# Kernel tuning notes

Hardware: AMD Instinct MI355X
Metric: run time of the kernel (lower is better)

## Reference

```python
import jax, jax.numpy as jnp
import numpy as np

N_NODES = 100000
N_EDGES = 1600000
NUM_FEATURES = 128
DIM = 64
NUM_GRAPHS = 64


def setup_inputs() -> dict:
    key = jax.random.key(0)
    ks = jax.random.split(key, 8)
    x = jax.random.normal(ks[0], (N_NODES, NUM_FEATURES), dtype=jnp.float32)
    edge_index = jax.random.randint(ks[1], (2, N_EDGES), 0, N_NODES, dtype=jnp.int64)
    batch = jnp.sort(jax.random.randint(ks[2], (N_NODES,), 0, NUM_GRAPHS, dtype=jnp.int64))
    s = 1.0 / np.sqrt(NUM_FEATURES)
    w_lin0 = jax.random.uniform(ks[3], (NUM_FEATURES, DIM), jnp.float32, -s, s)
    b_lin0 = jnp.zeros((DIM,), jnp.float32)
    s2 = 1.0 / np.sqrt(DIM)
    w0 = jax.random.uniform(ks[4], (DIM, DIM), jnp.float32, -s2, s2)
    w1 = jax.random.uniform(ks[5], (DIM, DIM), jnp.float32, -s2, s2)
    b_cheb = jnp.zeros((DIM,), jnp.float32)
    return {"x": x, "edge_index": edge_index, "batch": batch,
            "w_lin0": w_lin0, "b_lin0": b_lin0, "w0": w0, "w1": w1, "b_cheb": b_cheb}


def reference(x, edge_index, batch, w_lin0, b_lin0, w0, w1, b_cheb):
    # out = relu(lin0(x))
    out = jax.nn.relu(x @ w_lin0 + b_lin0)  # [N, DIM]

    src, dst = edge_index[0], edge_index[1]
    n = out.shape[0]
    # ChebConv K=2, sym normalization, lambda_max=2 (PyG default):
    # scaled Laplacian L_hat = L - I = -D^{-1/2} A D^{-1/2} (diagonal cancels to 0)
    deg = jax.ops.segment_sum(jnp.ones(src.shape, out.dtype), src, num_segments=n)
    dinv = jnp.where(deg > 0, 1.0 / jnp.sqrt(jnp.where(deg > 0, deg, 1.0)), 0.0)
    norm = -dinv[src] * dinv[dst]  # [E]

    tx0 = out
    # Tx_1 = L_hat @ x : gather source features, scale, scatter-add to targets
    tx1 = jax.ops.segment_sum(norm[:, None] * out[src], dst, num_segments=n)  # [N, DIM]

    h = jax.nn.relu(tx0 @ w0 + tx1 @ w1 + b_cheb)  # [N, DIM]

    pooled = jax.ops.segment_sum(h, batch, num_segments=NUM_GRAPHS)  # [G, DIM]
    return pooled, h
```

## Files before the change

### kernel.cpp

```cpp
#include <hip/hip_runtime.h>
#include <hip/hip_bf16.h>

#define N_NODES     100000
#define N_EDGES     1600000
#define NFEAT       128
#define DIM         64
#define NGRAPHS     64

#define CAP         64

#define ROWS_PB     32
#define NB_ROWS     ((N_NODES + ROWS_PB - 1) / ROWS_PB)

__device__ __forceinline__ float bf2f(unsigned short u) {
    return __uint_as_float(((unsigned)u) << 16);
}
__device__ __forceinline__ unsigned short f2bf(float f) {
    unsigned u = __float_as_uint(f);
    u += 0x7fffu + ((u >> 16) & 1u);
    return (unsigned short)(u >> 16);
}

__global__ __launch_bounds__(256) void init_kernel(
    int* __restrict__ deg, int* __restrict__ cursor, float* __restrict__ pooled)
{
    int i = blockIdx.x * 256 + threadIdx.x;
    if (i < N_NODES) {
        deg[i] = 0;
        cursor[i] = i * CAP;
    }
    if (i < NGRAPHS * DIM) pooled[i] = 0.0f;
}

__global__ __launch_bounds__(256) void lin0_kernel(
    const float* __restrict__ x, const float* __restrict__ w,
    const float* __restrict__ b, unsigned short* __restrict__ tx0b)
{
    __shared__ float wl[NFEAT * DIM];
    for (int i = threadIdx.x; i < NFEAT * DIM; i += 256) wl[i] = w[i];
    __syncthreads();

    const int lane = threadIdx.x & 63;
    const int wv   = threadIdx.x >> 6;
    const int r0   = blockIdx.x * ROWS_PB + wv * 8;
    if (r0 >= N_NODES) return;
    const float bv = b[lane];

    float acc[8];
#pragma unroll
    for (int j = 0; j < 8; ++j) acc[j] = bv;

    for (int k4 = 0; k4 < NFEAT / 4; ++k4) {
        const int k = k4 * 4;
        float4 xv[8];
#pragma unroll
        for (int j = 0; j < 8; ++j)
            xv[j] = *(const float4*)(x + (size_t)(r0 + j) * NFEAT + k);
        float w0v = wl[(k + 0) * DIM + lane];
        float w1v = wl[(k + 1) * DIM + lane];
        float w2v = wl[(k + 2) * DIM + lane];
        float w3v = wl[(k + 3) * DIM + lane];
#pragma unroll
        for (int j = 0; j < 8; ++j) {
            acc[j] = fmaf(xv[j].x, w0v, acc[j]);
            acc[j] = fmaf(xv[j].y, w1v, acc[j]);
            acc[j] = fmaf(xv[j].z, w2v, acc[j]);
            acc[j] = fmaf(xv[j].w, w3v, acc[j]);
        }
    }
#pragma unroll
    for (int j = 0; j < 8; ++j)
        tx0b[(size_t)(r0 + j) * DIM + lane] = f2bf(fmaxf(acc[j], 0.0f));
}

__global__ __launch_bounds__(256) void csr_deg_kernel(
    const int* __restrict__ ei, int* __restrict__ deg,
    int* __restrict__ cursor, int* __restrict__ csr_src)
{
    int e = blockIdx.x * 256 + threadIdx.x;
    if (e >= N_EDGES) return;
    int s = ei[e];
    int d = ei[N_EDGES + e];
    atomicAdd(&deg[s], 1);
    int pos = atomicAdd(&cursor[d], 1);
    if (pos < d * CAP + CAP)
        csr_src[pos] = s;
}

__global__ __launch_bounds__(256) void gather_kernel(
    const int* __restrict__ csr_src, const int* __restrict__ cursor,
    const int* __restrict__ deg, const unsigned short* __restrict__ tx0b,
    unsigned short* __restrict__ tx1b)
{
    int node = blockIdx.x * 4 + (threadIdx.x >> 6);
    if (node >= N_NODES) return;
    int lane = threadIdx.x & 63;
    int sub  = lane >> 4;
    int q    = lane & 15;

    int beg = node * CAP;
    int end = cursor[node];
    if (end > beg + CAP) end = beg + CAP;

    float4 acc = make_float4(0.f, 0.f, 0.f, 0.f);
    int p = beg + sub;
    for (; p + 4 < end; p += 8) {
        int s0 = csr_src[p];
        int s1 = csr_src[p + 4];
        float d0 = rsqrtf((float)deg[s0]);
        float d1 = rsqrtf((float)deg[s1]);
        ushort4 v0 = *(const ushort4*)(tx0b + (size_t)s0 * DIM + q * 4);
        ushort4 v1 = *(const ushort4*)(tx0b + (size_t)s1 * DIM + q * 4);
        acc.x = fmaf(d0, bf2f(v0.x), acc.x);
        acc.y = fmaf(d0, bf2f(v0.y), acc.y);
        acc.z = fmaf(d0, bf2f(v0.z), acc.z);
        acc.w = fmaf(d0, bf2f(v0.w), acc.w);
        acc.x = fmaf(d1, bf2f(v1.x), acc.x);
        acc.y = fmaf(d1, bf2f(v1.y), acc.y);
        acc.z = fmaf(d1, bf2f(v1.z), acc.z);
        acc.w = fmaf(d1, bf2f(v1.w), acc.w);
    }
    if (p < end) {
        int s = csr_src[p];
        float ds = rsqrtf((float)deg[s]);
        ushort4 v = *(const ushort4*)(tx0b + (size_t)s * DIM + q * 4);
        acc.x = fmaf(ds, bf2f(v.x), acc.x);
        acc.y = fmaf(ds, bf2f(v.y), acc.y);
        acc.z = fmaf(ds, bf2f(v.z), acc.z);
        acc.w = fmaf(ds, bf2f(v.w), acc.w);
    }
#pragma unroll
    for (int off = 16; off <= 32; off <<= 1) {
        acc.x += __shfl_xor(acc.x, off, 64);
        acc.y += __shfl_xor(acc.y, off, 64);
        acc.z += __shfl_xor(acc.z, off, 64);
        acc.w += __shfl_xor(acc.w, off, 64);
    }
    if (sub == 0) {
        int dg = deg[node];
        float nd = (dg > 0) ? -rsqrtf((float)dg) : 0.0f;
        ushort4 r;
        r.x = f2bf(nd * acc.x);
        r.y = f2bf(nd * acc.y);
        r.z = f2bf(nd * acc.z);
        r.w = f2bf(nd * acc.w);
        *(ushort4*)(tx1b + (size_t)node * DIM + q * 4) = r;
    }
}

__global__ __launch_bounds__(256) void cheb_kernel(
    const unsigned short* __restrict__ tx0b, const unsigned short* __restrict__ tx1b,
    const float* __restrict__ w0, const float* __restrict__ w1,
    const float* __restrict__ b, const int* __restrict__ batch,
    float* __restrict__ pooled, float* __restrict__ h)
{
    __shared__ float w0l[DIM * DIM];
    __shared__ float w1l[DIM * DIM];
    for (int i = threadIdx.x; i < DIM * DIM; i += 256) {
        w0l[i] = w0[i];
        w1l[i] = w1[i];
    }
    __syncthreads();

    const int lane = threadIdx.x & 63;
    const int wv   = threadIdx.x >> 6;
    const int r0   = blockIdx.x * ROWS_PB + wv * 8;
    if (r0 >= N_NODES) return;
    const float bv = b[lane];

    float acc[8];
#pragma unroll
    for (int j = 0; j < 8; ++j) acc[j] = bv;

    for (int k4 = 0; k4 < DIM / 4; ++k4) {
        const int k = k4 * 4;
        float a0 = w0l[(k + 0) * DIM + lane];
        float a1 = w0l[(k + 1) * DIM + lane];
        float a2 = w0l[(k + 2) * DIM + lane];
        float a3 = w0l[(k + 3) * DIM + lane];
        float c0 = w1l[(k + 0) * DIM + lane];
        float c1 = w1l[(k + 1) * DIM + lane];
        float c2 = w1l[(k + 2) * DIM + lane];
        float c3 = w1l[(k + 3) * DIM + lane];
#pragma unroll
        for (int j = 0; j < 8; ++j) {
            ushort4 t0 = *(const ushort4*)(tx0b + (size_t)(r0 + j) * DIM + k);
            ushort4 t1 = *(const ushort4*)(tx1b + (size_t)(r0 + j) * DIM + k);
            acc[j] = fmaf(bf2f(t0.x), a0, acc[j]);
            acc[j] = fmaf(bf2f(t0.y), a1, acc[j]);
            acc[j] = fmaf(bf2f(t0.z), a2, acc[j]);
            acc[j] = fmaf(bf2f(t0.w), a3, acc[j]);
            acc[j] = fmaf(bf2f(t1.x), c0, acc[j]);
            acc[j] = fmaf(bf2f(t1.y), c1, acc[j]);
            acc[j] = fmaf(bf2f(t1.z), c2, acc[j]);
            acc[j] = fmaf(bf2f(t1.w), c3, acc[j]);
        }
    }

    float acc_pool = 0.0f;
    int cur_g = -1;
#pragma unroll
    for (int j = 0; j < 8; ++j) {
        float hv = fmaxf(acc[j], 0.0f);
        h[(size_t)(r0 + j) * DIM + lane] = hv;
        int g = batch[r0 + j];
        if (g != cur_g) {
            if (cur_g >= 0) unsafeAtomicAdd(&pooled[cur_g * DIM + lane], acc_pool);
            cur_g = g;
            acc_pool = 0.0f;
        }
        acc_pool += hv;
    }
    if (cur_g >= 0) unsafeAtomicAdd(&pooled[cur_g * DIM + lane], acc_pool);
}

extern "C" void kernel_launch(void* const* d_in, const int* in_sizes, int n_in,
                              void* d_out, int out_size, void* d_ws, size_t ws_size,
                              hipStream_t stream)
{
    const float* x      = (const float*)d_in[0];
    const int*   ei     = (const int*)d_in[1];
    const int*   batch  = (const int*)d_in[2];
    const float* w_lin0 = (const float*)d_in[3];
    const float* b_lin0 = (const float*)d_in[4];
    const float* w0     = (const float*)d_in[5];
    const float* w1     = (const float*)d_in[6];
    const float* b_cheb = (const float*)d_in[7];

    float* pooled = (float*)d_out;
    float* h      = (float*)d_out + NGRAPHS * DIM;

    char* wp = (char*)d_ws;
    unsigned short* tx0b = (unsigned short*)wp; wp += (size_t)N_NODES * DIM * sizeof(unsigned short);
    unsigned short* tx1b = (unsigned short*)wp; wp += (size_t)N_NODES * DIM * sizeof(unsigned short);
    int* deg     = (int*)wp;  wp += (size_t)N_NODES * sizeof(int);
    int* cursor  = (int*)wp;  wp += (size_t)N_NODES * sizeof(int);
    int* csr_src = (int*)wp;  wp += (size_t)N_NODES * CAP * sizeof(int);

    init_kernel<<<(N_NODES + 255) / 256, 256, 0, stream>>>(deg, cursor, pooled);

    lin0_kernel<<<NB_ROWS, 256, 0, stream>>>(x, w_lin0, b_lin0, tx0b);

    csr_deg_kernel<<<(N_EDGES + 255) / 256, 256, 0, stream>>>(ei, deg, cursor, csr_src);

    gather_kernel<<<(N_NODES + 3) / 4, 256, 0, stream>>>(csr_src, cursor, deg, tx0b, tx1b);

    cheb_kernel<<<NB_ROWS, 256, 0, stream>>>(tx0b, tx1b, w0, w1, b_cheb,
                                             batch, pooled, h);
}
```

Baseline: 517.5 us.

## Prescale tx0 by source dinv and widen gather loads to 16 bytes

A new pass multiplies each tx0 row in place by rsqrt(deg) of its source node. The gather then sums prescaled rows without reading deg[src] or doing an rsqrt per edge, and uses 16-byte loads with 8 lanes per neighbor row. The cheb kernel splits its accumulators and multiplies the tx0 part by sqrt(deg) to undo the scaling. This adds an extra read-write pass over tx0 and a second bf16 rounding of the scaled values, which could cost some accuracy.

```diff
diff --git a/kernel.cpp b/kernel.cpp
--- a/kernel.cpp
+++ b/kernel.cpp
@@ -11,6 +11,8 @@
 
 #define ROWS_PB     32
 #define NB_ROWS     ((N_NODES + ROWS_PB - 1) / ROWS_PB)
+
+typedef unsigned short ushort8v __attribute__((ext_vector_type(8)));
 
 __device__ __forceinline__ float bf2f(unsigned short u) {
     return __uint_as_float(((unsigned)u) << 16);
@@ -87,69 +89,73 @@
         csr_src[pos] = s;
 }
 
+__global__ __launch_bounds__(256) void scale_kernel(
+    const int* __restrict__ deg, unsigned short* __restrict__ tx0b)
+{
+    int t = blockIdx.x * 256 + threadIdx.x;
+    if (t >= N_NODES * DIM / 8) return;
+    int node = t >> 3;
+    int dg = deg[node];
+    float f = (dg > 0) ? rsqrtf((float)dg) : 1.0f;
+    ushort8v v = *(((const ushort8v*)tx0b) + t);
+#pragma unroll
+    for (int k = 0; k < 8; ++k) v[k] = f2bf(f * bf2f(v[k]));
+    *(((ushort8v*)tx0b) + t) = v;
+}
+
 __global__ __launch_bounds__(256) void gather_kernel(
     const int* __restrict__ csr_src, const int* __restrict__ cursor,
-    const int* __restrict__ deg, const unsigned short* __restrict__ tx0b,
+    const int* __restrict__ deg, const unsigned short* __restrict__ tx0s,
     unsigned short* __restrict__ tx1b)
 {
     int node = blockIdx.x * 4 + (threadIdx.x >> 6);
     if (node >= N_NODES) return;
     int lane = threadIdx.x & 63;
-    int sub  = lane >> 4;
-    int q    = lane & 15;
+    int sub  = lane >> 3;
+    int q    = lane & 7;
 
     int beg = node * CAP;
     int end = cursor[node];
     if (end > beg + CAP) end = beg + CAP;
 
-    float4 acc = make_float4(0.f, 0.f, 0.f, 0.f);
+    float acc[8];
+#pragma unroll
+    for (int k = 0; k < 8; ++k) acc[k] = 0.0f;
+
     int p = beg + sub;
-    for (; p + 4 < end; p += 8) {
+    for (; p + 8 < end; p += 16) {
         int s0 = csr_src[p];
-        int s1 = csr_src[p + 4];
-        float d0 = rsqrtf((float)deg[s0]);
-        float d1 = rsqrtf((float)deg[s1]);
-        ushort4 v0 = *(const ushort4*)(tx0b + (size_t)s0 * DIM + q * 4);
-        ushort4 v1 = *(const ushort4*)(tx0b + (size_t)s1 * DIM + q * 4);
-        acc.x = fmaf(d0, bf2f(v0.x), acc.x);
-        acc.y = fmaf(d0, bf2f(v0.y), acc.y);
-        acc.z = fmaf(d0, bf2f(v0.z), acc.z);
-        acc.w = fmaf(d0, bf2f(v0.w), acc.w);
-        acc.x = fmaf(d1, bf2f(v1.x), acc.x);
-        acc.y = fmaf(d1, bf2f(v1.y), acc.y);
-        acc.z = fmaf(d1, bf2f(v1.z), acc.z);
-        acc.w = fmaf(d1, bf2f(v1.w), acc.w);
+        int s1 = csr_src[p + 8];
+        ushort8v v0 = *(const ushort8v*)(tx0s + (size_t)s0 * DIM + q * 8);
+        ushort8v v1 = *(const ushort8v*)(tx0s + (size_t)s1 * DIM + q * 8);
+#pragma unroll
+        for (int k = 0; k < 8; ++k) acc[k] += bf2f(v0[k]) + bf2f(v1[k]);
     }
     if (p < end) {
         int s = csr_src[p];
-        float ds = rsqrtf((float)deg[s]);
-        ushort4 v = *(const ushort4*)(tx0b + (size_t)s * DIM + q * 4);
-        acc.x = fmaf(ds, bf2f(v.x), acc.x);
-        acc.y = fmaf(ds, bf2f(v.y), acc.y);
-        acc.z = fmaf(ds, bf2f(v.z), acc.z);
-        acc.w = fmaf(ds, bf2f(v.w), acc.w);
-    }
-#pragma unroll
-    for (int off = 16; off <= 32; off <<= 1) {
-        acc.x += __shfl_xor(acc.x, off, 64);
-        acc.y += __shfl_xor(acc.y, off, 64);
-        acc.z += __shfl_xor(acc.z, off, 64);
-        acc.w += __shfl_xor(acc.w, off, 64);
+        ushort8v v = *(const ushort8v*)(tx0s + (size_t)s * DIM + q * 8);
+#pragma unroll
+        for (int k = 0; k < 8; ++k) acc[k] += bf2f(v[k]);
+    }
+#pragma unroll
+    for (int off = 8; off <= 32; off <<= 1) {
+#pragma unroll
+        for (int k = 0; k < 8; ++k)
+            acc[k] += __shfl_xor(acc[k], off, 64);
     }
     if (sub == 0) {
         int dg = deg[node];
         float nd = (dg > 0) ? -rsqrtf((float)dg) : 0.0f;
-        ushort4 r;
-        r.x = f2bf(nd * acc.x);
-        r.y = f2bf(nd * acc.y);
-        r.z = f2bf(nd * acc.z);
-        r.w = f2bf(nd * acc.w);
-        *(ushort4*)(tx1b + (size_t)node * DIM + q * 4) = r;
+        ushort8v r;
+#pragma unroll
+        for (int k = 0; k < 8; ++k) r[k] = f2bf(nd * acc[k]);
+        *(ushort8v*)(tx1b + (size_t)node * DIM + q * 8) = r;
     }
 }
 
 __global__ __launch_bounds__(256) void cheb_kernel(
-    const unsigned short* __restrict__ tx0b, const unsigned short* __restrict__ tx1b,
+    const unsigned short* __restrict__ tx0s, const unsigned short* __restrict__ tx1b,
+    const int* __restrict__ deg,
     const float* __restrict__ w0, const float* __restrict__ w1,
     const float* __restrict__ b, const int* __restrict__ batch,
     float* __restrict__ pooled, float* __restrict__ h)
@@ -168,9 +174,9 @@
     if (r0 >= N_NODES) return;
     const float bv = b[lane];
 
-    float acc[8];
-#pragma unroll
-    for (int j = 0; j < 8; ++j) acc[j] = bv;
+    float accA[8], accB[8];
+#pragma unroll
+    for (int j = 0; j < 8; ++j) { accA[j] = 0.0f; accB[j] = 0.0f; }
 
     for (int k4 = 0; k4 < DIM / 4; ++k4) {
         const int k = k4 * 4;
@@ -184,16 +190,16 @@
         float c3 = w1l[(k + 3) * DIM + lane];
 #pragma unroll
         for (int j = 0; j < 8; ++j) {
-            ushort4 t0 = *(const ushort4*)(tx0b + (size_t)(r0 + j) * DIM + k);
+            ushort4 t0 = *(const ushort4*)(tx0s + (size_t)(r0 + j) * DIM + k);
             ushort4 t1 = *(const ushort4*)(tx1b + (size_t)(r0 + j) * DIM + k);
-            acc[j] = fmaf(bf2f(t0.x), a0, acc[j]);
-            acc[j] = fmaf(bf2f(t0.y), a1, acc[j]);
-            acc[j] = fmaf(bf2f(t0.z), a2, acc[j]);
-            acc[j] = fmaf(bf2f(t0.w), a3, acc[j]);
-            acc[j] = fmaf(bf2f(t1.x), c0, acc[j]);
-            acc[j] = fmaf(bf2f(t1.y), c1, acc[j]);
-            acc[j] = fmaf(bf2f(t1.z), c2, acc[j]);
-            acc[j] = fmaf(bf2f(t1.w), c3, acc[j]);
+            accA[j] = fmaf(bf2f(t0.x), a0, accA[j]);
+            accA[j] = fmaf(bf2f(t0.y), a1, accA[j]);
+            accA[j] = fmaf(bf2f(t0.z), a2, accA[j]);
+            accA[j] = fmaf(bf2f(t0.w), a3, accA[j]);
+            accB[j] = fmaf(bf2f(t1.x), c0, accB[j]);
+            accB[j] = fmaf(bf2f(t1.y), c1, accB[j]);
+            accB[j] = fmaf(bf2f(t1.z), c2, accB[j]);
+            accB[j] = fmaf(bf2f(t1.w), c3, accB[j]);
         }
     }
 
@@ -201,7 +207,9 @@
     int cur_g = -1;
 #pragma unroll
     for (int j = 0; j < 8; ++j) {
-        float hv = fmaxf(acc[j], 0.0f);
+        int dg = deg[r0 + j];
+        float sq = (dg > 0) ? sqrtf((float)dg) : 1.0f;
+        float hv = fmaxf(fmaf(sq, accA[j], accB[j] + bv), 0.0f);
         h[(size_t)(r0 + j) * DIM + lane] = hv;
         int g = batch[r0 + j];
         if (g != cur_g) {
@@ -243,8 +251,10 @@
 
     csr_deg_kernel<<<(N_EDGES + 255) / 256, 256, 0, stream>>>(ei, deg, cursor, csr_src);
 
+    scale_kernel<<<(N_NODES * DIM / 8 + 255) / 256, 256, 0, stream>>>(deg, tx0b);
+
     gather_kernel<<<(N_NODES + 3) / 4, 256, 0, stream>>>(csr_src, cursor, deg, tx0b, tx1b);
 
-    cheb_kernel<<<NB_ROWS, 256, 0, stream>>>(tx0b, tx1b, w0, w1, b_cheb,
+    cheb_kernel<<<NB_ROWS, 256, 0, stream>>>(tx0b, tx1b, deg, w0, w1, b_cheb,
                                              batch, pooled, h);
 }
```

Result: no change. 518.9 us (+0.3%).
